# Kernel tuning notes

Measured on AMD Instinct MI355X. Metric: run time of the kernel, lower is better.

The kernel has to match this reference:

```python
import jax, jax.numpy as jnp
import numpy as np

N, E = 50000, 400000
D_IN, D_H, N_CLS = 256, 64, 50
BN_EPS = 1e-5


def _gat_layer(x, src, dst, W, att_s, att_d, bias, heads, out_c, concat):
    # x: [N, in]; W: [in, heads*out_c]; att_s/att_d: [heads, out_c]
    n = x.shape[0]
    h = (x @ W).reshape(n, heads, out_c)                       # [N,H,C]
    a_s = jnp.einsum('nhc,hc->nh', h, att_s)                   # [N,H]
    a_d = jnp.einsum('nhc,hc->nh', h, att_d)
    e = jax.nn.leaky_relu(a_s[src] + a_d[dst], 0.2)            # [E',H]
    emax = jax.lax.stop_gradient(jax.ops.segment_max(e, dst, num_segments=n))
    emax = jnp.where(jnp.isfinite(emax), emax, 0.0)
    p = jnp.exp(e - emax[dst])
    denom = jax.ops.segment_sum(p, dst, num_segments=n)
    alpha = p / (denom[dst] + 1e-16)                           # segment softmax over in-edges of dst
    out = jax.ops.segment_sum(h[src] * alpha[:, :, None], dst, num_segments=n)  # [N,H,C]
    out = out.reshape(n, heads * out_c) if concat else out.mean(axis=1)
    return out + bias


def _bn_eval(x, g, b, rm, rv):
    return (x - rm) * g * jax.lax.rsqrt(rv + BN_EPS) + b


def setup_inputs() -> dict:
    key = jax.random.key(0)
    ks = jax.random.split(key, 24)
    s = lambda i, shape: jax.random.normal(ks[i], shape, dtype=jnp.float32) * 0.05
    inp = {
        'x': jax.random.normal(ks[0], (N, D_IN), dtype=jnp.float32),
        'edge_index': jax.random.randint(ks[1], (2, E), 0, N, dtype=jnp.int64),
        # GAT layer 1: heads=8, concat=False
        'W1': s(2, (D_IN, 8 * D_H)), 'as1': s(3, (8, D_H)), 'ad1': s(4, (8, D_H)), 'b1': s(5, (D_H,)),
        # GAT layer 2: heads=4, concat=False
        'W2': s(6, (D_H, 4 * D_H)), 'as2': s(7, (4, D_H)), 'ad2': s(8, (4, D_H)), 'b2': s(9, (D_H,)),
        # GAT layer 3: heads=1, concat=True
        'W3': s(10, (D_H, D_H)), 'as3': s(11, (1, D_H)), 'ad3': s(12, (1, D_H)), 'b3': s(13, (D_H,)),
        # BatchNorm (eval mode, running stats)
        'bn1_g': jnp.ones((D_H,), jnp.float32), 'bn1_b': jnp.zeros((D_H,), jnp.float32),
        'bn1_m': s(14, (D_H,)), 'bn1_v': jax.random.uniform(ks[15], (D_H,), jnp.float32) + 0.5,
        'bn2_g': jnp.ones((D_H,), jnp.float32), 'bn2_b': jnp.zeros((D_H,), jnp.float32),
        'bn2_m': s(16, (D_H,)), 'bn2_v': jax.random.uniform(ks[17], (D_H,), jnp.float32) + 0.5,
        # topic classifier
        'cW1': s(18, (D_H, D_H)), 'cb1': s(19, (D_H,)),
        'cW2': s(20, (D_H, N_CLS)), 'cb2': s(21, (N_CLS,)),
    }
    return inp


def reference(x, edge_index, W1, as1, ad1, b1, W2, as2, ad2, b2, W3, as3, ad3, b3,
              bn1_g, bn1_b, bn1_m, bn1_v, bn2_g, bn2_b, bn2_m, bn2_v,
              cW1, cb1, cW2, cb2):
    n = x.shape[0]
    loops = jnp.arange(n, dtype=edge_index.dtype)
    src = jnp.concatenate([edge_index[0], loops])   # add_self_loops=True (PyG default)
    dst = jnp.concatenate([edge_index[1], loops])

    h = _gat_layer(x, src, dst, W1, as1, ad1, b1, heads=8, out_c=D_H, concat=False)
    h = jax.nn.relu(_bn_eval(h, bn1_g, bn1_b, bn1_m, bn1_v))
    h = _gat_layer(h, src, dst, W2, as2, ad2, b2, heads=4, out_c=D_H, concat=False)
    h = jax.nn.relu(_bn_eval(h, bn2_g, bn2_b, bn2_m, bn2_v))
    h = _gat_layer(h, src, dst, W3, as3, ad3, b3, heads=1, out_c=D_H, concat=True)

    z = jax.nn.relu(h @ cW1 + cb1)
    logits = z @ cW2 + cb2
    return jax.nn.softmax(logits, axis=-1)
```

## Files before the change

### kernel.cpp

```cpp
#include <hip/hip_runtime.h>
#include <hip/hip_bf16.h>
#include <math.h>

#define NN 50000
#define EE 400000
#define D_IN 256
#define D_H 64
#define N_CLS 50

typedef __attribute__((ext_vector_type(8))) short bfrag;
typedef __attribute__((ext_vector_type(4))) float ffrag;
typedef __attribute__((ext_vector_type(8))) unsigned short u16x8_t;
typedef __attribute__((ext_vector_type(4))) unsigned short u16x4_t;

__device__ __forceinline__ unsigned short f2bf(float v) {
    unsigned int u = __float_as_uint(v);
    unsigned int r = (u + 0x7fffu + ((u >> 16) & 1u)) >> 16;
    return (unsigned short)r;
}
__device__ __forceinline__ float bf2f(unsigned short b) {
    return __uint_as_float(((unsigned int)b) << 16);
}

__device__ __forceinline__ int swz(int row, int q) {
    return row * 32 + ((q ^ ((row >> 1) & 3)) << 3);
}

__global__ void zero_k(int* p, int n) {
    int i = blockIdx.x * blockDim.x + threadIdx.x;
    if (i < n) p[i] = 0;
}

__global__ void count_k(const int* __restrict__ ei, int* __restrict__ cnt, int E, int N) {
    int i = blockIdx.x * blockDim.x + threadIdx.x;
    if (i >= E + N) return;
    int dst = (i < E) ? ei[E + i] : (i - E);
    atomicAdd(&cnt[dst], 1);
}

__global__ __launch_bounds__(1024) void scan1_k(const int* __restrict__ counts,
                                                int* __restrict__ excl,
                                                int* __restrict__ bsum, int n) {
    __shared__ int wsum[16];
    int t = threadIdx.x;
    int lane = t & 63, wid = t >> 6;
    int idx = blockIdx.x * 1024 + t;
    int v = (idx < n) ? counts[idx] : 0;
    int incl = v;
    #pragma unroll
    for (int off = 1; off < 64; off <<= 1) {
        int x = __shfl_up(incl, off);
        if (lane >= off) incl += x;
    }
    if (lane == 63) wsum[wid] = incl;
    __syncthreads();
    if (wid == 0) {
        int ws = (lane < 16) ? wsum[lane] : 0;
        int wincl = ws;
        #pragma unroll
        for (int off = 1; off < 16; off <<= 1) {
            int x = __shfl_up(wincl, off);
            if (lane >= off) wincl += x;
        }
        if (lane < 16) wsum[lane] = wincl - ws;
    }
    __syncthreads();
    if (idx < n) excl[idx] = wsum[wid] + (incl - v);
    if (t == 1023) bsum[blockIdx.x] = wsum[15] + incl;
}

__global__ void scan2_k(int* __restrict__ bsum, int nb) {
    int lane = threadIdx.x & 63;
    int v = (lane < nb) ? bsum[lane] : 0;
    int incl = v;
    #pragma unroll
    for (int off = 1; off < 64; off <<= 1) {
        int x = __shfl_up(incl, off);
        if (lane >= off) incl += x;
    }
    if (lane < nb) bsum[lane] = incl - v;
}

__global__ void scan3_k(const int* __restrict__ excl, const int* __restrict__ bsum,
                        int* __restrict__ rowptr, int n, int total) {
    int i = blockIdx.x * 256 + threadIdx.x;
    if (i < n) rowptr[i] = excl[i] + bsum[i >> 10];
    if (i == 0) rowptr[n] = total;
}

__global__ void fill_k(const int* __restrict__ ei, const int* __restrict__ rowptr,
                       int* __restrict__ cursor, int* __restrict__ csr, int E, int N) {
    int i = blockIdx.x * blockDim.x + threadIdx.x;
    if (i >= E + N) return;
    int s, d;
    if (i < E) { s = ei[i]; d = ei[E + i]; }
    else       { s = i - E; d = i - E; }
    int pos = atomicAdd(&cursor[d], 1);
    csr[rowptr[d] + pos] = s;
}

__global__ void cvt_a_k(const float* __restrict__ a, unsigned short* __restrict__ hi,
                        unsigned short* __restrict__ lo, int n) {
    int i = blockIdx.x * 256 + threadIdx.x;
    if (i >= n) return;
    float v = a[i];
    unsigned short h = f2bf(v);
    hi[i] = h;
    lo[i] = f2bf(v - bf2f(h));
}

__global__ void cvt_bt_k(const float* __restrict__ Bsrc, unsigned short* __restrict__ hi,
                         unsigned short* __restrict__ lo, int K, int N) {
    int i = blockIdx.x * 256 + threadIdx.x;
    if (i >= K * N) return;
    int k = i / N, n = i % N;
    float v = Bsrc[i];
    unsigned short h = f2bf(v);
    hi[(size_t)n * K + k] = h;
    lo[(size_t)n * K + k] = f2bf(v - bf2f(h));
}

__global__ void bnprep_k(const float* __restrict__ g, const float* __restrict__ b,
                         const float* __restrict__ m, const float* __restrict__ v,
                         const float* __restrict__ bias,
                         float* __restrict__ scale, float* __restrict__ shift) {
    int t = threadIdx.x;
    if (t < 64) {
        float sc = g[t] * rsqrtf(v[t] + 1e-5f);
        scale[t] = sc;
        shift[t] = (bias[t] - m[t]) * sc + b[t];
    }
}

__global__ __launch_bounds__(256) void gemm_mfma_k(
    const unsigned short* __restrict__ Ahi, const unsigned short* __restrict__ Alo,
    const unsigned short* __restrict__ BThi, const unsigned short* __restrict__ BTlo,
    float* __restrict__ Cf, unsigned short* __restrict__ Chi, unsigned short* __restrict__ Clo,
    int M, int N, int K,
    const float* __restrict__ bias, int do_relu,
    const float* __restrict__ att_s, const float* __restrict__ att_d,
    float* __restrict__ asb, float* __restrict__ adb, int H) {
    __shared__ unsigned short sAh[64 * 32];
    __shared__ unsigned short sAl[64 * 32];
    __shared__ unsigned short sBh[128 * 32];
    __shared__ unsigned short sBl[128 * 32];
    const int tid = threadIdx.x;
    const int m0 = blockIdx.y * 64;
    const int n0 = blockIdx.x * 128;
    const int lane = tid & 63, w = tid >> 6;
    const int wm = w >> 1, wn = w & 1;
    const int c16 = lane & 15, kq = lane >> 4;
    const int arow = tid >> 2;
    const int q    = tid & 3;
    const int akc  = q * 8;
    const int aM  = min(m0 + arow, M - 1);
    const int bn0 = min(n0 + arow, N - 1);
    const int bn1 = min(n0 + 64 + arow, N - 1);
    const int wA  = swz(arow, q);
    const int wB0 = swz(arow, q);
    const int wB1 = swz(64 + arow, q);
    ffrag acc[2][4] = {};

    for (int k0 = 0; k0 < K; k0 += 32) {
        bfrag va_h  = *(const bfrag*)(Ahi  + (size_t)aM  * K + k0 + akc);
        bfrag va_l  = *(const bfrag*)(Alo  + (size_t)aM  * K + k0 + akc);
        bfrag vb_h0 = *(const bfrag*)(BThi + (size_t)bn0 * K + k0 + akc);
        bfrag vb_l0 = *(const bfrag*)(BTlo + (size_t)bn0 * K + k0 + akc);
        bfrag vb_h1 = *(const bfrag*)(BThi + (size_t)bn1 * K + k0 + akc);
        bfrag vb_l1 = *(const bfrag*)(BTlo + (size_t)bn1 * K + k0 + akc);
        __syncthreads();
        *(bfrag*)&sAh[wA]  = va_h;
        *(bfrag*)&sAl[wA]  = va_l;
        *(bfrag*)&sBh[wB0] = vb_h0;
        *(bfrag*)&sBl[wB0] = vb_l0;
        *(bfrag*)&sBh[wB1] = vb_h1;
        *(bfrag*)&sBl[wB1] = vb_l1;
        __syncthreads();
        bfrag ah[2], al_[2], bh[4], bl[4];
        #pragma unroll
        for (int mt = 0; mt < 2; mt++) {
            int ra = wm * 32 + mt * 16 + c16;
            ah[mt]  = *(const bfrag*)&sAh[swz(ra, kq)];
            al_[mt] = *(const bfrag*)&sAl[swz(ra, kq)];
        }
        #pragma unroll
        for (int nt = 0; nt < 4; nt++) {
            int rb = wn * 64 + nt * 16 + c16;
            bh[nt] = *(const bfrag*)&sBh[swz(rb, kq)];
            bl[nt] = *(const bfrag*)&sBl[swz(rb, kq)];
        }
        #pragma unroll
        for (int mt = 0; mt < 2; mt++)
            #pragma unroll
            for (int nt = 0; nt < 4; nt++) {
                acc[mt][nt] = __builtin_amdgcn_mfma_f32_16x16x32_bf16(ah[mt],  bh[nt], acc[mt][nt], 0, 0, 0);
                acc[mt][nt] = __builtin_amdgcn_mfma_f32_16x16x32_bf16(ah[mt],  bl[nt], acc[mt][nt], 0, 0, 0);
                acc[mt][nt] = __builtin_amdgcn_mfma_f32_16x16x32_bf16(al_[mt], bh[nt], acc[mt][nt], 0, 0, 0);
            }
    }

    if (att_s) {
        int hidx = n0 / 64 + wn;
        if (hidx < H) {
            float s_att[4], d_att[4];
            #pragma unroll
            for (int nt = 0; nt < 4; nt++) {
                s_att[nt] = att_s[hidx * 64 + nt * 16 + c16];
                d_att[nt] = att_d[hidx * 64 + nt * 16 + c16];
            }
            #pragma unroll
            for (int mt = 0; mt < 2; mt++) {
                #pragma unroll
                for (int r = 0; r < 4; r++) {
                    int row = m0 + wm * 32 + mt * 16 + kq * 4 + r;
                    float ps = 0.f, pd = 0.f;
                    #pragma unroll
                    for (int nt = 0; nt < 4; nt++) {
                        ps = fmaf(acc[mt][nt][r], s_att[nt], ps);
                        pd = fmaf(acc[mt][nt][r], d_att[nt], pd);
                    }
                    #pragma unroll
                    for (int msk = 1; msk < 16; msk <<= 1) {
                        ps += __shfl_xor(ps, msk);
                        pd += __shfl_xor(pd, msk);
                    }
                    if (c16 == 0 && row < M) {
                        asb[(size_t)row * H + hidx] = ps;
                        adb[(size_t)row * H + hidx] = pd;
                    }
                }
            }
        }
    }

    #pragma unroll
    for (int mt = 0; mt < 2; mt++) {
        #pragma unroll
        for (int r = 0; r < 4; r++) {
            int row = m0 + wm * 32 + mt * 16 + kq * 4 + r;
            if (row < M) {
                #pragma unroll
                for (int nt = 0; nt < 4; nt++) {
                    int col = n0 + wn * 64 + nt * 16 + c16;
                    if (col < N) {
                        float v = acc[mt][nt][r];
                        if (bias) v += bias[col];
                        if (do_relu) v = fmaxf(v, 0.f);
                        size_t idx = (size_t)row * N + col;
                        if (Cf) Cf[idx] = v;
                        if (Chi) {
                            unsigned short hh = f2bf(v);
                            Chi[idx] = hh;
                            if (Clo) Clo[idx] = f2bf(v - bf2f(hh));
                        }
                    }
                }
            }
        }
    }
}

__device__ __forceinline__ float wave_max_f(float v) {
    #pragma unroll
    for (int off = 32; off; off >>= 1) v = fmaxf(v, __shfl_xor(v, off));
    return v;
}
__device__ __forceinline__ float wave_sum_f(float v) {
    #pragma unroll
    for (int off = 32; off; off >>= 1) v += __shfl_xor(v, off);
    return v;
}

template <int H, bool MEAN_BN>
__global__ __launch_bounds__(256) void agg_k(
    const unsigned short* __restrict__ hfeat,
    const float* __restrict__ a_s, const float* __restrict__ a_d,
    const int* __restrict__ rowptr, const int* __restrict__ csr,
    const float* __restrict__ scale,
    const float* __restrict__ shift,
    unsigned short* __restrict__ outhi, unsigned short* __restrict__ outlo,
    int N) {
    constexpr int OUT = H * 64;
    constexpr int F = H;
    constexpr int G = 64 / H;
    constexpr int EPC = 64 / H;
    __shared__ float alpha_s[4][H][65];
    __shared__ int srcb[4][64];
    const int wv = threadIdx.x >> 6;
    const int lane = threadIdx.x & 63;
    const int node = blockIdx.x * 4 + wv;
    if (node >= N) return;

    const int row = rowptr[node];
    const int deg = rowptr[node + 1] - row;
    const int hl = lane / G;

    float acc[F] = {};
    float inv = 1.f;

    if (deg <= 64) {
        const int j8 = lane / H;
        const int h8 = lane % H;
        float adn_own = a_d[(size_t)node * H + h8];
        float psum = 0.f;
        for (int c0 = 0; c0 < deg; c0 += EPC) {
            int jj = c0 + j8;
            if (jj < deg) {
                int s = csr[row + jj];
                if (h8 == 0) srcb[wv][jj] = s;
                float e = a_s[(size_t)s * H + h8] + adn_own;
                e = e > 0.f ? e : 0.2f * e;
                float p = __expf(e);
                alpha_s[wv][h8][jj] = p;
                psum += p;
            }
        }
        #pragma unroll
        for (int msk = H; msk < 64; msk <<= 1)
            psum += __shfl_xor(psum, msk);
        float invd = 1.f / (psum + 1e-16f);
        inv = __shfl(invd, hl);
        asm volatile("s_waitcnt lgkmcnt(0)" ::: "memory");
        for (int jj = 0; jj < deg; jj++) {
            int ss = srcb[wv][jj];
            float al = alpha_s[wv][hl][jj];
            const unsigned short* rp = hfeat + (size_t)ss * OUT + lane * F;
            if constexpr (F == 8) {
                u16x8_t u = *(const u16x8_t*)rp;
                #pragma unroll
                for (int i = 0; i < 8; i++) acc[i] = fmaf(al, bf2f(u[i]), acc[i]);
            } else if constexpr (F == 4) {
                u16x4_t u = *(const u16x4_t*)rp;
                #pragma unroll
                for (int i = 0; i < 4; i++) acc[i] = fmaf(al, bf2f(u[i]), acc[i]);
            } else {
                acc[0] = fmaf(al, bf2f(rp[0]), acc[0]);
            }
        }
    } else {
        float adn[H];
        #pragma unroll
        for (int h = 0; h < H; h++) adn[h] = a_d[(size_t)node * H + h];
        float m[H];
        #pragma unroll
        for (int h = 0; h < H; h++) m[h] = -INFINITY;
        for (int c0 = 0; c0 < deg; c0 += 64) {
            int j = c0 + lane;
            if (j < deg) {
                int s2 = csr[row + j];
                #pragma unroll
                for (int h = 0; h < H; h++) {
                    float e = a_s[(size_t)s2 * H + h] + adn[h];
                    e = e > 0.f ? e : 0.2f * e;
                    m[h] = fmaxf(m[h], e);
                }
            }
        }
        #pragma unroll
        for (int h = 0; h < H; h++) m[h] = wave_max_f(m[h]);
        float dsum[H] = {};
        for (int c0 = 0; c0 < deg; c0 += 64) {
            int j = c0 + lane;
            if (j < deg) {
                int s2 = csr[row + j];
                #pragma unroll
                for (int h = 0; h < H; h++) {
                    float e = a_s[(size_t)s2 * H + h] + adn[h];
                    e = e > 0.f ? e : 0.2f * e;
                    dsum[h] += __expf(e - m[h]);
                }
            }
        }
        float dinv[H];
        #pragma unroll
        for (int h = 0; h < H; h++) dinv[h] = 1.f / (wave_sum_f(dsum[h]) + 1e-16f);
        for (int c0 = 0; c0 < deg; c0 += 64) {
            int j = c0 + lane;
            int cnt = min(64, deg - c0);
            int s = 0;
            if (j < deg) {
                s = csr[row + j];
                #pragma unroll
                for (int h = 0; h < H; h++) {
                    float e = a_s[(size_t)s * H + h] + adn[h];
                    e = e > 0.f ? e : 0.2f * e;
                    alpha_s[wv][h][lane] = __expf(e - m[h]) * dinv[h];
                }
            }
            asm volatile("s_waitcnt lgkmcnt(0)" ::: "memory");
            for (int jj = 0; jj < cnt; jj++) {
                int ss = __builtin_amdgcn_readlane(s, jj);
                float al = alpha_s[wv][hl][jj];
                const unsigned short* rp = hfeat + (size_t)ss * OUT + lane * F;
                if constexpr (F == 8) {
                    u16x8_t u = *(const u16x8_t*)rp;
                    #pragma unroll
                    for (int i = 0; i < 8; i++) acc[i] = fmaf(al, bf2f(u[i]), acc[i]);
                } else if constexpr (F == 4) {
                    u16x4_t u = *(const u16x4_t*)rp;
                    #pragma unroll
                    for (int i = 0; i < 4; i++) acc[i] = fmaf(al, bf2f(u[i]), acc[i]);
                } else {
                    acc[0] = fmaf(al, bf2f(rp[0]), acc[0]);
                }
            }
            asm volatile("s_waitcnt lgkmcnt(0)" ::: "memory");
        }
        inv = 1.f;
    }

    #pragma unroll
    for (int i = 0; i < F; i++) acc[i] *= inv;

    if constexpr (MEAN_BN) {
        #pragma unroll
        for (int i = 0; i < F; i++) {
            #pragma unroll
            for (int msk = G; msk < 64; msk <<= 1)
                acc[i] += __shfl_xor(acc[i], msk);
        }
        if (lane < G) {
            int c0 = lane * F;
            #pragma unroll
            for (int i = 0; i < F; i++) {
                float v = fmaf(acc[i] * (1.0f / H), scale[c0 + i], shift[c0 + i]);
                v = fmaxf(v, 0.f);
                unsigned short hh = f2bf(v);
                outhi[(size_t)node * 64 + c0 + i] = hh;
                outlo[(size_t)node * 64 + c0 + i] = f2bf(v - bf2f(hh));
            }
        }
    } else {
        float v = acc[0] + shift[lane];
        unsigned short hh = f2bf(v);
        outhi[(size_t)node * 64 + lane] = hh;
        outlo[(size_t)node * 64 + lane] = f2bf(v - bf2f(hh));
    }
}

__global__ __launch_bounds__(256) void softmax_k(const float* __restrict__ logits,
                                                 float* __restrict__ out, int N) {
    int lane = threadIdx.x & 63;
    int n = (blockIdx.x * blockDim.x + threadIdx.x) >> 6;
    if (n >= N) return;
    float lg = (lane < N_CLS) ? logits[(size_t)n * N_CLS + lane] : -INFINITY;
    float m = wave_max_f(lg);
    float p = (lane < N_CLS) ? __expf(lg - m) : 0.f;
    float s = wave_sum_f(p);
    if (lane < N_CLS) out[(size_t)n * N_CLS + lane] = p / s;
}

extern "C" void kernel_launch(void* const* d_in, const int* in_sizes, int n_in,
                              void* d_out, int out_size, void* d_ws, size_t ws_size,
                              hipStream_t stream) {
    const int N = NN, E = EE, E2 = EE + NN;
    const float* x    = (const float*)d_in[0];
    const int*   ei   = (const int*)d_in[1];
    const float* W1   = (const float*)d_in[2];
    const float* as1  = (const float*)d_in[3];
    const float* ad1  = (const float*)d_in[4];
    const float* b1   = (const float*)d_in[5];
    const float* W2   = (const float*)d_in[6];
    const float* as2  = (const float*)d_in[7];
    const float* ad2  = (const float*)d_in[8];
    const float* b2   = (const float*)d_in[9];
    const float* W3   = (const float*)d_in[10];
    const float* as3  = (const float*)d_in[11];
    const float* ad3  = (const float*)d_in[12];
    const float* b3   = (const float*)d_in[13];
    const float* bn1g = (const float*)d_in[14];
    const float* bn1b = (const float*)d_in[15];
    const float* bn1m = (const float*)d_in[16];
    const float* bn1v = (const float*)d_in[17];
    const float* bn2g = (const float*)d_in[18];
    const float* bn2b = (const float*)d_in[19];
    const float* bn2m = (const float*)d_in[20];
    const float* bn2v = (const float*)d_in[21];
    const float* cW1  = (const float*)d_in[22];
    const float* cb1  = (const float*)d_in[23];
    const float* cW2  = (const float*)d_in[24];
    const float* cb2  = (const float*)d_in[25];
    float* out = (float*)d_out;

    char* ws = (char*)d_ws;
    size_t off = 0;
    auto alloc = [&](size_t bytes) {
        void* p = ws + off;
        off = (off + bytes + 255) & ~(size_t)255;
        return p;
    };
    int*   rowptr = (int*)alloc((size_t)(N + 1) * 4);
    int*   cursor = (int*)alloc((size_t)N * 4);
    int*   excl   = (int*)alloc((size_t)N * 4);
    int*   bsum   = (int*)alloc(64 * 4);
    int*   csr    = (int*)alloc((size_t)E2 * 4);
    unsigned short* hbf = (unsigned short*)alloc((size_t)N * 512 * 2);
    float* asb    = (float*)alloc((size_t)N * 8 * 4);
    float* adb    = (float*)alloc((size_t)N * 8 * 4);
    unsigned short* xhi = (unsigned short*)alloc((size_t)N * D_IN * 2);
    unsigned short* xlo = (unsigned short*)alloc((size_t)N * D_IN * 2);
    unsigned short* f1h = (unsigned short*)alloc((size_t)N * 64 * 2);
    unsigned short* f1l = (unsigned short*)alloc((size_t)N * 64 * 2);
    unsigned short* f2h = (unsigned short*)alloc((size_t)N * 64 * 2);
    unsigned short* f2l = (unsigned short*)alloc((size_t)N * 64 * 2);
    unsigned short* f3h = (unsigned short*)alloc((size_t)N * 64 * 2);
    unsigned short* f3l = (unsigned short*)alloc((size_t)N * 64 * 2);
    unsigned short* zh  = (unsigned short*)alloc((size_t)N * 64 * 2);
    unsigned short* zl  = (unsigned short*)alloc((size_t)N * 64 * 2);
    unsigned short* wthi = (unsigned short*)alloc((size_t)512 * 256 * 2);
    unsigned short* wtlo = (unsigned short*)alloc((size_t)512 * 256 * 2);
    float* sc1 = (float*)alloc(64 * 4);
    float* sh1 = (float*)alloc(64 * 4);
    float* sc2 = (float*)alloc(64 * 4);
    float* sh2 = (float*)alloc(64 * 4);
    float* logits = (float*)alloc((size_t)N * N_CLS * 4);

    const int NB = (N + 1023) / 1024;

    zero_k<<<(N + 255) / 256, 256, 0, stream>>>(cursor, N);
    count_k<<<(E2 + 255) / 256, 256, 0, stream>>>(ei, cursor, E, N);
    scan1_k<<<NB, 1024, 0, stream>>>(cursor, excl, bsum, N);
    scan2_k<<<1, 64, 0, stream>>>(bsum, NB);
    scan3_k<<<(N + 255) / 256, 256, 0, stream>>>(excl, bsum, rowptr, N, E2);
    zero_k<<<(N + 255) / 256, 256, 0, stream>>>(cursor, N);
    fill_k<<<(E2 + 255) / 256, 256, 0, stream>>>(ei, rowptr, cursor, csr, E, N);
    bnprep_k<<<1, 64, 0, stream>>>(bn1g, bn1b, bn1m, bn1v, b1, sc1, sh1);
    bnprep_k<<<1, 64, 0, stream>>>(bn2g, bn2b, bn2m, bn2v, b2, sc2, sh2);

    const int MB = (N + 63) / 64;
    const int AB = (N + 3) / 4;

    cvt_a_k<<<((size_t)N * 256 + 255) / 256, 256, 0, stream>>>(x, xhi, xlo, N * 256);
    cvt_bt_k<<<(256 * 512 + 255) / 256, 256, 0, stream>>>(W1, wthi, wtlo, 256, 512);
    gemm_mfma_k<<<dim3(4, MB), 256, 0, stream>>>(xhi, xlo, wthi, wtlo,
        nullptr, hbf, nullptr, N, 512, 256, nullptr, 0, as1, ad1, asb, adb, 8);
    agg_k<8, true><<<AB, 256, 0, stream>>>(hbf, asb, adb, rowptr, csr, sc1, sh1, f1h, f1l, N);

    cvt_bt_k<<<(64 * 256 + 255) / 256, 256, 0, stream>>>(W2, wthi, wtlo, 64, 256);
    gemm_mfma_k<<<dim3(2, MB), 256, 0, stream>>>(f1h, f1l, wthi, wtlo,
        nullptr, hbf, nullptr, N, 256, 64, nullptr, 0, as2, ad2, asb, adb, 4);
    agg_k<4, true><<<AB, 256, 0, stream>>>(hbf, asb, adb, rowptr, csr, sc2, sh2, f2h, f2l, N);

    cvt_bt_k<<<(64 * 64 + 255) / 256, 256, 0, stream>>>(W3, wthi, wtlo, 64, 64);
    gemm_mfma_k<<<dim3(1, MB), 256, 0, stream>>>(f2h, f2l, wthi, wtlo,
        nullptr, hbf, nullptr, N, 64, 64, nullptr, 0, as3, ad3, asb, adb, 1);
    agg_k<1, false><<<AB, 256, 0, stream>>>(hbf, asb, adb, rowptr, csr, nullptr, b3, f3h, f3l, N);

    cvt_bt_k<<<(64 * 64 + 255) / 256, 256, 0, stream>>>(cW1, wthi, wtlo, 64, 64);
    gemm_mfma_k<<<dim3(1, MB), 256, 0, stream>>>(f3h, f3l, wthi, wtlo,
        nullptr, zh, zl, N, 64, 64, cb1, 1, nullptr, nullptr, nullptr, nullptr, 0);
    cvt_bt_k<<<(64 * N_CLS + 255) / 256, 256, 0, stream>>>(cW2, wthi, wtlo, 64, N_CLS);
    gemm_mfma_k<<<dim3(1, MB), 256, 0, stream>>>(zh, zl, wthi, wtlo,
        logits, nullptr, nullptr, N, N_CLS, 64, cb2, 0, nullptr, nullptr, nullptr, nullptr, 0);
    softmax_k<<<(N + 3) / 4, 256, 0, stream>>>(logits, out, N);
}
```

Measured before the change: 497.5 us.

## Fold layer-3 GAT projection into classifier weights and fuse x conversion into GEMM

```diff
diff --git a/kernel.cpp b/kernel.cpp
--- a/kernel.cpp
+++ b/kernel.cpp
@@ -99,16 +99,6 @@
     csr[rowptr[d] + pos] = s;
 }
 
-__global__ void cvt_a_k(const float* __restrict__ a, unsigned short* __restrict__ hi,
-                        unsigned short* __restrict__ lo, int n) {
-    int i = blockIdx.x * 256 + threadIdx.x;
-    if (i >= n) return;
-    float v = a[i];
-    unsigned short h = f2bf(v);
-    hi[i] = h;
-    lo[i] = f2bf(v - bf2f(h));
-}
-
 __global__ void cvt_bt_k(const float* __restrict__ Bsrc, unsigned short* __restrict__ hi,
                          unsigned short* __restrict__ lo, int K, int N) {
     int i = blockIdx.x * 256 + threadIdx.x;
@@ -132,7 +122,34 @@
     }
 }
 
+__global__ void prep3_k(const float* __restrict__ W3, const float* __restrict__ cW1,
+                        const float* __restrict__ as3, const float* __restrict__ ad3,
+                        const float* __restrict__ b3, const float* __restrict__ cb1,
+                        float* __restrict__ Wc, float* __restrict__ w_as3,
+                        float* __restrict__ w_ad3, float* __restrict__ bc) {
+    int j = blockIdx.x;
+    int i = threadIdx.x;
+    float s = 0.f;
+    for (int k = 0; k < 64; k++) s += W3[i * 64 + k] * cW1[k * 64 + j];
+    Wc[i * 64 + j] = s;
+    if (j == 0) {
+        float sa = 0.f, sd = 0.f;
+        for (int c = 0; c < 64; c++) {
+            sa += W3[i * 64 + c] * as3[c];
+            sd += W3[i * 64 + c] * ad3[c];
+        }
+        w_as3[i] = sa;
+        w_ad3[i] = sd;
+    }
+    if (i == 0) {
+        float s2 = 0.f;
+        for (int k = 0; k < 64; k++) s2 += b3[k] * cW1[k * 64 + j];
+        bc[j] = s2 + cb1[j];
+    }
+}
+
 __global__ __launch_bounds__(256) void gemm_mfma_k(
+    const float* __restrict__ Af,
     const unsigned short* __restrict__ Ahi, const unsigned short* __restrict__ Alo,
     const unsigned short* __restrict__ BThi, const unsigned short* __restrict__ BTlo,
     float* __restrict__ Cf, unsigned short* __restrict__ Chi, unsigned short* __restrict__ Clo,
@@ -159,15 +176,35 @@
     const int wA  = swz(arow, q);
     const int wB0 = swz(arow, q);
     const int wB1 = swz(64 + arow, q);
+    const float* pAf          = Af  ? Af  + (size_t)aM * K + akc : nullptr;
+    const unsigned short* pAh = Ahi ? Ahi + (size_t)aM * K + akc : nullptr;
+    const unsigned short* pAl = Alo ? Alo + (size_t)aM * K + akc : nullptr;
+    const unsigned short* pBh0 = BThi + (size_t)bn0 * K + akc;
+    const unsigned short* pBl0 = BTlo + (size_t)bn0 * K + akc;
+    const unsigned short* pBh1 = BThi + (size_t)bn1 * K + akc;
+    const unsigned short* pBl1 = BTlo + (size_t)bn1 * K + akc;
     ffrag acc[2][4] = {};
 
     for (int k0 = 0; k0 < K; k0 += 32) {
-        bfrag va_h  = *(const bfrag*)(Ahi  + (size_t)aM  * K + k0 + akc);
-        bfrag va_l  = *(const bfrag*)(Alo  + (size_t)aM  * K + k0 + akc);
-        bfrag vb_h0 = *(const bfrag*)(BThi + (size_t)bn0 * K + k0 + akc);
-        bfrag vb_l0 = *(const bfrag*)(BTlo + (size_t)bn0 * K + k0 + akc);
-        bfrag vb_h1 = *(const bfrag*)(BThi + (size_t)bn1 * K + k0 + akc);
-        bfrag vb_l1 = *(const bfrag*)(BTlo + (size_t)bn1 * K + k0 + akc);
+        bfrag va_h, va_l;
+        if (Af) {
+            float4 f0 = *(const float4*)(pAf + k0);
+            float4 f1 = *(const float4*)(pAf + k0 + 4);
+            float fv[8] = {f0.x, f0.y, f0.z, f0.w, f1.x, f1.y, f1.z, f1.w};
+            #pragma unroll
+            for (int i = 0; i < 8; i++) {
+                unsigned short hh = f2bf(fv[i]);
+                va_h[i] = (short)hh;
+                va_l[i] = (short)f2bf(fv[i] - bf2f(hh));
+            }
+        } else {
+            va_h = *(const bfrag*)(pAh + k0);
+            va_l = *(const bfrag*)(pAl + k0);
+        }
+        bfrag vb_h0 = *(const bfrag*)(pBh0 + k0);
+        bfrag vb_l0 = *(const bfrag*)(pBl0 + k0);
+        bfrag vb_h1 = *(const bfrag*)(pBh1 + k0);
+        bfrag vb_l1 = *(const bfrag*)(pBl1 + k0);
         __syncthreads();
         *(bfrag*)&sAh[wA]  = va_h;
         *(bfrag*)&sAl[wA]  = va_l;
@@ -279,6 +316,8 @@
     const float* __restrict__ scale,
     const float* __restrict__ shift,
     unsigned short* __restrict__ outhi, unsigned short* __restrict__ outlo,
+    const float* __restrict__ was3, const float* __restrict__ wad3,
+    float* __restrict__ as3o, float* __restrict__ ad3o,
     int N) {
     constexpr int OUT = H * 64;
     constexpr int F = H;
@@ -419,22 +458,47 @@
             for (int msk = G; msk < 64; msk <<= 1)
                 acc[i] += __shfl_xor(acc[i], msk);
         }
+        const int c0 = (lane < G) ? lane * F : 0;
+        float res[F];
         if (lane < G) {
-            int c0 = lane * F;
             #pragma unroll
             for (int i = 0; i < F; i++) {
                 float v = fmaf(acc[i] * (1.0f / H), scale[c0 + i], shift[c0 + i]);
-                v = fmaxf(v, 0.f);
-                unsigned short hh = f2bf(v);
+                res[i] = fmaxf(v, 0.f);
+            }
+        } else {
+            #pragma unroll
+            for (int i = 0; i < F; i++) res[i] = 0.f;
+        }
+        if (was3) {
+            float ps = 0.f, pd = 0.f;
+            if (lane < G) {
+                #pragma unroll
+                for (int i = 0; i < F; i++) {
+                    ps = fmaf(res[i], was3[c0 + i], ps);
+                    pd = fmaf(res[i], wad3[c0 + i], pd);
+                }
+            }
+            #pragma unroll
+            for (int msk = 1; msk < G; msk <<= 1) {
+                ps += __shfl_xor(ps, msk);
+                pd += __shfl_xor(pd, msk);
+            }
+            if (lane == 0) { as3o[node] = ps; ad3o[node] = pd; }
+        }
+        if (lane < G) {
+            #pragma unroll
+            for (int i = 0; i < F; i++) {
+                unsigned short hh = f2bf(res[i]);
                 outhi[(size_t)node * 64 + c0 + i] = hh;
-                outlo[(size_t)node * 64 + c0 + i] = f2bf(v - bf2f(hh));
+                if (outlo) outlo[(size_t)node * 64 + c0 + i] = f2bf(res[i] - bf2f(hh));
             }
         }
     } else {
-        float v = acc[0] + shift[lane];
+        float v = acc[0] + (shift ? shift[lane] : 0.f);
         unsigned short hh = f2bf(v);
         outhi[(size_t)node * 64 + lane] = hh;
-        outlo[(size_t)node * 64 + lane] = f2bf(v - bf2f(hh));
+        if (outlo) outlo[(size_t)node * 64 + lane] = f2bf(v - bf2f(hh));
     }
 }
 
@@ -497,12 +561,11 @@
     unsigned short* hbf = (unsigned short*)alloc((size_t)N * 512 * 2);
     float* asb    = (float*)alloc((size_t)N * 8 * 4);
     float* adb    = (float*)alloc((size_t)N * 8 * 4);
-    unsigned short* xhi = (unsigned short*)alloc((size_t)N * D_IN * 2);
-    unsigned short* xlo = (unsigned short*)alloc((size_t)N * D_IN * 2);
+    float* as3b   = (float*)alloc((size_t)N * 4);
+    float* ad3b   = (float*)alloc((size_t)N * 4);
     unsigned short* f1h = (unsigned short*)alloc((size_t)N * 64 * 2);
     unsigned short* f1l = (unsigned short*)alloc((size_t)N * 64 * 2);
     unsigned short* f2h = (unsigned short*)alloc((size_t)N * 64 * 2);
-    unsigned short* f2l = (unsigned short*)alloc((size_t)N * 64 * 2);
     unsigned short* f3h = (unsigned short*)alloc((size_t)N * 64 * 2);
     unsigned short* f3l = (unsigned short*)alloc((size_t)N * 64 * 2);
     unsigned short* zh  = (unsigned short*)alloc((size_t)N * 64 * 2);
@@ -513,6 +576,10 @@
     float* sh1 = (float*)alloc(64 * 4);
     float* sc2 = (float*)alloc(64 * 4);
     float* sh2 = (float*)alloc(64 * 4);
+    float* Wc    = (float*)alloc(64 * 64 * 4);
+    float* w_as3 = (float*)alloc(64 * 4);
+    float* w_ad3 = (float*)alloc(64 * 4);
+    float* bc    = (float*)alloc(64 * 4);
     float* logits = (float*)alloc((size_t)N * N_CLS * 4);
 
     const int NB = (N + 1023) / 1024;
@@ -526,31 +593,31 @@
     fill_k<<<(E2 + 255) / 256, 256, 0, stream>>>(ei, rowptr, cursor, csr, E, N);
     bnprep_k<<<1, 64, 0, stream>>>(bn1g, bn1b, bn1m, bn1v, b1, sc1, sh1);
     bnprep_k<<<1, 64, 0, stream>>>(bn2g, bn2b, bn2m, bn2v, b2, sc2, sh2);
+    prep3_k<<<64, 64, 0, stream>>>(W3, cW1, as3, ad3, b3, cb1, Wc, w_as3, w_ad3, bc);
 
     const int MB = (N + 63) / 64;
     const int AB = (N + 3) / 4;
 
-    cvt_a_k<<<((size_t)N * 256 + 255) / 256, 256, 0, stream>>>(x, xhi, xlo, N * 256);
     cvt_bt_k<<<(256 * 512 + 255) / 256, 256, 0, stream>>>(W1, wthi, wtlo, 256, 512);
-    gemm_mfma_k<<<dim3(4, MB), 256, 0, stream>>>(xhi, xlo, wthi, wtlo,
+    gemm_mfma_k<<<dim3(4, MB), 256, 0, stream>>>(x, nullptr, nullptr, wthi, wtlo,
         nullptr, hbf, nullptr, N, 512, 256, nullptr, 0, as1, ad1, asb, adb, 8);
-    agg_k<8, true><<<AB, 256, 0, stream>>>(hbf, asb, adb, rowptr, csr, sc1, sh1, f1h, f1l, N);
+    agg_k<8, true><<<AB, 256, 0, stream>>>(hbf, asb, adb, rowptr, csr, sc1, sh1,
+        f1h, f1l, nullptr, nullptr, nullptr, nullptr, N);
 
     cvt_bt_k<<<(64 * 256 + 255) / 256, 256, 0, stream>>>(W2, wthi, wtlo, 64, 256);
-    gemm_mfma_k<<<dim3(2, MB), 256, 0, stream>>>(f1h, f1l, wthi, wtlo,
+    gemm_mfma_k<<<dim3(2, MB), 256, 0, stream>>>(nullptr, f1h, f1l, wthi, wtlo,
         nullptr, hbf, nullptr, N, 256, 64, nullptr, 0, as2, ad2, asb, adb, 4);
-    agg_k<4, true><<<AB, 256, 0, stream>>>(hbf, asb, adb, rowptr, csr, sc2, sh2, f2h, f2l, N);
-
-    cvt_bt_k<<<(64 * 64 + 255) / 256, 256, 0, stream>>>(W3, wthi, wtlo, 64, 64);
-    gemm_mfma_k<<<dim3(1, MB), 256, 0, stream>>>(f2h, f2l, wthi, wtlo,
-        nullptr, hbf, nullptr, N, 64, 64, nullptr, 0, as3, ad3, asb, adb, 1);
-    agg_k<1, false><<<AB, 256, 0, stream>>>(hbf, asb, adb, rowptr, csr, nullptr, b3, f3h, f3l, N);
-
-    cvt_bt_k<<<(64 * 64 + 255) / 256, 256, 0, stream>>>(cW1, wthi, wtlo, 64, 64);
-    gemm_mfma_k<<<dim3(1, MB), 256, 0, stream>>>(f3h, f3l, wthi, wtlo,
-        nullptr, zh, zl, N, 64, 64, cb1, 1, nullptr, nullptr, nullptr, nullptr, 0);
+    agg_k<4, true><<<AB, 256, 0, stream>>>(hbf, asb, adb, rowptr, csr, sc2, sh2,
+        f2h, nullptr, w_as3, w_ad3, as3b, ad3b, N);
+
+    agg_k<1, false><<<AB, 256, 0, stream>>>(f2h, as3b, ad3b, rowptr, csr, nullptr, nullptr,
+        f3h, f3l, nullptr, nullptr, nullptr, nullptr, N);
+    cvt_bt_k<<<(64 * 64 + 255) / 256, 256, 0, stream>>>(Wc, wthi, wtlo, 64, 64);
+    gemm_mfma_k<<<dim3(1, MB), 256, 0, stream>>>(nullptr, f3h, f3l, wthi, wtlo,
+        nullptr, zh, zl, N, 64, 64, bc, 1, nullptr, nullptr, nullptr, nullptr, 0);
+
     cvt_bt_k<<<(64 * N_CLS + 255) / 256, 256, 0, stream>>>(cW2, wthi, wtlo, 64, N_CLS);
-    gemm_mfma_k<<<dim3(1, MB), 256, 0, stream>>>(zh, zl, wthi, wtlo,
+    gemm_mfma_k<<<dim3(1, MB), 256, 0, stream>>>(nullptr, zh, zl, wthi, wtlo,
         logits, nullptr, nullptr, N, N_CLS, 64, cb2, 0, nullptr, nullptr, nullptr, nullptr, 0);
     softmax_k<<<(N + 3) / 4, 256, 0, stream>>>(logits, out, N);
 }
```

Result: faster. 468.1 us (-5.9%).
